# Kernel tuning notes

Hardware: AMD Instinct MI355X
Metric: run time of the kernel (lower is better)

## Reference

```python
import jax, jax.numpy as jnp
import numpy as np

DIM = 768
N_HEADS = 12
HEAD_DIM = DIM // N_HEADS
B, S = 16, 1024


def setup_inputs() -> dict:
    key = jax.random.key(0)
    k1, k2, k3, k4, k5 = jax.random.split(key, 5)
    scale = 0.02
    return {
        "x": jax.random.normal(k1, (B, S, DIM), dtype=jnp.float32),
        "W_attn": jax.random.normal(k2, (DIM, 3 * DIM), dtype=jnp.float32) * scale,
        "b_attn": jnp.zeros((3 * DIM,), dtype=jnp.float32),
        "W_proj": jax.random.normal(k3, (DIM, DIM), dtype=jnp.float32) * scale,
        "b_proj": jnp.zeros((DIM,), dtype=jnp.float32),
    }


def reference(x, W_attn, b_attn, W_proj, b_proj):
    # Dropout layers act as identity (eval mode) for a deterministic reference.
    Bsz, Sq, D = x.shape
    qkv = x @ W_attn + b_attn                      # [B, S, 3D]
    q, k, v = jnp.split(qkv, 3, axis=-1)
    q = q.reshape(Bsz, Sq, N_HEADS, HEAD_DIM)
    k = k.reshape(Bsz, Sq, N_HEADS, HEAD_DIM)
    v = v.reshape(Bsz, Sq, N_HEADS, HEAD_DIM)
    # scores: [B, H, S, S]
    w = jnp.einsum('bqhd,bkhd->bhqk', q, k) / jnp.sqrt(jnp.float32(HEAD_DIM))
    causal = jnp.tril(jnp.ones((Sq, Sq), dtype=bool))
    mask_value = jnp.finfo(w.dtype).min
    w = jnp.where(causal[None, None], w, mask_value)
    w = jax.nn.softmax(w, axis=-1)
    attn = jnp.einsum('bhqk,bkhd->bqhd', w, v).reshape(Bsz, Sq, D)
    return attn @ W_proj + b_proj
```

## Files before the change

### kernel.cpp

```cpp
#include <hip/hip_runtime.h>
#include <hip/hip_bf16.h>
#include <math.h>

#define BDIM 16
#define SEQ 1024
#define DIM 768
#define NH 12
#define HD 64
#define M_ROWS (BDIM * SEQ)
#define N_QKV (3 * DIM)
#define QN (BDIM * NH * SEQ * HD)

typedef __attribute__((ext_vector_type(8))) short bf16x8_t;
typedef __attribute__((ext_vector_type(4))) float f32x4_t;
typedef __attribute__((ext_vector_type(16))) float f32x16_t;
typedef __attribute__((ext_vector_type(4))) unsigned int u32x4_t;

__device__ __forceinline__ unsigned short f2bf(float x) {
    return __builtin_bit_cast(unsigned short, __float2bfloat16(x));
}

__device__ __forceinline__ void gld_lds16(const void* g, void* l) {
    __builtin_amdgcn_global_load_lds(
        (const __attribute__((address_space(1))) void*)g,
        (__attribute__((address_space(3))) void*)l, 16, 0, 0);
}

__device__ __forceinline__ unsigned int cvt_pk_bf16(float a, float b) {
    unsigned int r;
    asm("v_cvt_pk_bf16_f32 %0, %1, %2" : "=v"(r) : "v"(a), "v"(b));
    return r;
}

__device__ __forceinline__ void perm32swap(unsigned int& a, unsigned int& b) {
    asm("v_permlane32_swap_b32 %0, %1" : "+v"(a), "+v"(b));
}

#define QSCALE 0.18033688011112042f

#define X_BLOCKS 6144
#define WA_TILES 432
#define WP_TILES 144

__global__ __launch_bounds__(256) void prep(
    const float* __restrict__ x, const float* __restrict__ Wa,
    const float* __restrict__ Wp,
    unsigned short* __restrict__ xb, unsigned short* __restrict__ Wat,
    unsigned short* __restrict__ Wpt)
{
    __shared__ unsigned short T[64][72];
    const int bid = blockIdx.x;
    const int tid = threadIdx.x;

    if (bid < X_BLOCKS) {
        size_t base = (size_t)bid * 2048 + tid * 8;
        float4 f0 = *(const float4*)&x[base];
        float4 f1 = *(const float4*)&x[base + 4];
        unsigned short tmp[8] = {f2bf(f0.x), f2bf(f0.y), f2bf(f0.z), f2bf(f0.w),
                                 f2bf(f1.x), f2bf(f1.y), f2bf(f1.z), f2bf(f1.w)};
        *(uint4*)&xb[base] = *(uint4*)tmp;
        return;
    }
    const float* W; unsigned short* Wt; int N, kt, nt;
    int b2 = bid - X_BLOCKS;
    if (b2 < WA_TILES) { W = Wa; Wt = Wat; N = N_QKV; kt = b2 / 36; nt = b2 % 36; }
    else { b2 -= WA_TILES; W = Wp; Wt = Wpt; N = DIM; kt = b2 / 12; nt = b2 % 12; }
    const int k0 = kt * 64, n0 = nt * 64;
#pragma unroll
    for (int c = 0; c < 4; c++) {
        int idx = c * 256 + tid;
        int r = idx >> 4;
        int c4 = (idx & 15) * 4;
        float4 v = *(const float4*)&W[(size_t)(k0 + r) * N + n0 + c4];
        T[r][c4 + 0] = f2bf(v.x);
        T[r][c4 + 1] = f2bf(v.y);
        T[r][c4 + 2] = f2bf(v.z);
        T[r][c4 + 3] = f2bf(v.w);
    }
    __syncthreads();
#pragma unroll
    for (int c = 0; c < 2; c++) {
        int idx = c * 256 + tid;
        int n = idx >> 3;
        int ch = (idx & 7) * 8;
        unsigned short tmp[8];
#pragma unroll
        for (int j = 0; j < 8; j++) tmp[j] = T[ch + j][n];
        *(uint4*)&Wt[(size_t)(n0 + n) * DIM + k0 + ch] = *(uint4*)tmp;
    }
}

__global__ __launch_bounds__(256, 2) void gemm_qkv_mfma(
    const unsigned short* __restrict__ Ab,
    const unsigned short* __restrict__ Bt,
    const float* __restrict__ bias,
    unsigned short* __restrict__ Qo, unsigned short* __restrict__ Ko,
    unsigned short* __restrict__ Vt)
{
    __shared__ unsigned short smem[32768];

    const int tid = threadIdx.x;
    const int lane = tid & 63;
    const int w = tid >> 6;
    const int wm = w >> 1, wn = w & 1;
    const int ln = lane & 15, quad = lane >> 4;
    const int bm = blockIdx.y * 128, bn = blockIdx.x * 128;

    f32x4_t acc[4][4];
#pragma unroll
    for (int i = 0; i < 4; i++)
#pragma unroll
        for (int j = 0; j < 4; j++) acc[i][j] = (f32x4_t){0.f, 0.f, 0.f, 0.f};

#pragma unroll
    for (int c = 0; c < 4; c++) {
        int idx = c * 256 + tid;
        int r = idx >> 3;
        int gch = (idx & 7) ^ (r & 7);
        gld_lds16(&Ab[(size_t)(bm + r) * DIM + gch * 8], &smem[idx * 8]);
        gld_lds16(&Bt[(size_t)(bn + r) * DIM + gch * 8], &smem[8192 + idx * 8]);
    }

    for (int ki = 0; ki < 12; ki++) {
        __syncthreads();
        unsigned short* As = smem + (ki & 1) * 16384;
        unsigned short* Bs = As + 8192;

        if (ki < 11) {
            const int nk0 = (ki + 1) * 64;
            unsigned short* Asn = smem + ((ki + 1) & 1) * 16384;
            unsigned short* Bsn = Asn + 8192;
#pragma unroll
            for (int c = 0; c < 4; c++) {
                int idx = c * 256 + tid;
                int r = idx >> 3;
                int gch = (idx & 7) ^ (r & 7);
                gld_lds16(&Ab[(size_t)(bm + r) * DIM + nk0 + gch * 8], &Asn[idx * 8]);
                gld_lds16(&Bt[(size_t)(bn + r) * DIM + nk0 + gch * 8], &Bsn[idx * 8]);
            }
        }

#pragma unroll
        for (int kk = 0; kk < 2; kk++) {
            bf16x8_t af[4], bfr[4];
#pragma unroll
            for (int mt = 0; mt < 4; mt++) {
                int r = wm * 64 + mt * 16 + ln;
                int c = (kk * 4 + quad) ^ (ln & 7);
                af[mt] = *(const bf16x8_t*)&As[r * 64 + c * 8];
            }
#pragma unroll
            for (int nt = 0; nt < 4; nt++) {
                int r = wn * 64 + nt * 16 + ln;
                int c = (kk * 4 + quad) ^ (ln & 7);
                bfr[nt] = *(const bf16x8_t*)&Bs[r * 64 + c * 8];
            }
#pragma unroll
            for (int mt = 0; mt < 4; mt++)
#pragma unroll
                for (int nt = 0; nt < 4; nt++)
                    acc[mt][nt] = __builtin_amdgcn_mfma_f32_16x16x32_bf16(
                        af[mt], bfr[nt], acc[mt][nt], 0, 0, 0);
        }
    }
    __syncthreads();

    const int nb = bn + wn * 64;
    const int part = nb / DIM;
    const int h = (nb % DIM) >> 6;
    const float scale = (part == 0) ? QSCALE : 1.0f;
    const int mb = bm + wm * 64;
    const int b_ = mb >> 10;
    const int s0 = mb & 1023;
    unsigned short* Wb = smem + w * 4608;

    float bias_v[4];
#pragma unroll
    for (int nt = 0; nt < 4; nt++) bias_v[nt] = bias[nb + nt * 16 + ln];

    if (part < 2) {
#pragma unroll
        for (int mt = 0; mt < 4; mt++)
#pragma unroll
            for (int nt = 0; nt < 4; nt++)
#pragma unroll
                for (int r = 0; r < 4; r++)
                    Wb[(mt * 16 + quad * 4 + r) * 72 + nt * 16 + ln] =
                        f2bf((acc[mt][nt][r] + bias_v[nt]) * scale);
        unsigned short* dst = (part == 0) ? Qo : Ko;
        size_t obase = (((size_t)b_ * NH + h) * SEQ + s0) * HD;
#pragma unroll
        for (int c = 0; c < 8; c++) {
            int idx = c * 64 + lane;
            int rr = idx >> 3;
            int ch = (idx & 7) * 8;
            *(uint4*)&dst[obase + (size_t)rr * HD + ch] = *(uint4*)&Wb[rr * 72 + ch];
        }
    } else {
#pragma unroll
        for (int mt = 0; mt < 4; mt++)
#pragma unroll
            for (int nt = 0; nt < 4; nt++)
#pragma unroll
                for (int r = 0; r < 4; r++)
                    Wb[(nt * 16 + ln) * 72 + mt * 16 + quad * 4 + r] =
                        f2bf(acc[mt][nt][r] + bias_v[nt]);
        size_t obase = ((size_t)b_ * NH + h) * (size_t)HD * SEQ;
#pragma unroll
        for (int c = 0; c < 8; c++) {
            int idx = c * 64 + lane;
            int d = idx >> 3;
            int ch = (idx & 7) * 8;
            *(uint4*)&Vt[obase + (size_t)d * SEQ + s0 + ch] = *(uint4*)&Wb[d * 72 + ch];
        }
    }
}

__global__ __launch_bounds__(256, 2) void gemm_proj_mfma(
    const unsigned short* __restrict__ Ab,
    const unsigned short* __restrict__ Bt,
    const float* __restrict__ bias,
    float* __restrict__ C)
{
    __shared__ unsigned short smem[32768];

    const int tid = threadIdx.x;
    const int lane = tid & 63;
    const int w = tid >> 6;
    const int wm = w >> 1, wn = w & 1;
    const int ln = lane & 15, quad = lane >> 4;
    const int bm = blockIdx.y * 128, bn = blockIdx.x * 128;

    f32x4_t acc[4][4];
#pragma unroll
    for (int i = 0; i < 4; i++)
#pragma unroll
        for (int j = 0; j < 4; j++) acc[i][j] = (f32x4_t){0.f, 0.f, 0.f, 0.f};

#pragma unroll
    for (int c = 0; c < 4; c++) {
        int idx = c * 256 + tid;
        int r = idx >> 3;
        int gch = (idx & 7) ^ (r & 7);
        gld_lds16(&Ab[(size_t)(bm + r) * DIM + gch * 8], &smem[idx * 8]);
        gld_lds16(&Bt[(size_t)(bn + r) * DIM + gch * 8], &smem[8192 + idx * 8]);
    }

    for (int ki = 0; ki < 12; ki++) {
        __syncthreads();
        unsigned short* As = smem + (ki & 1) * 16384;
        unsigned short* Bs = As + 8192;

        if (ki < 11) {
            const int nk0 = (ki + 1) * 64;
            unsigned short* Asn = smem + ((ki + 1) & 1) * 16384;
            unsigned short* Bsn = Asn + 8192;
#pragma unroll
            for (int c = 0; c < 4; c++) {
                int idx = c * 256 + tid;
                int r = idx >> 3;
                int gch = (idx & 7) ^ (r & 7);
                gld_lds16(&Ab[(size_t)(bm + r) * DIM + nk0 + gch * 8], &Asn[idx * 8]);
                gld_lds16(&Bt[(size_t)(bn + r) * DIM + nk0 + gch * 8], &Bsn[idx * 8]);
            }
        }

#pragma unroll
        for (int kk = 0; kk < 2; kk++) {
            bf16x8_t af[4], bfr[4];
#pragma unroll
            for (int mt = 0; mt < 4; mt++) {
                int r = wm * 64 + mt * 16 + ln;
                int c = (kk * 4 + quad) ^ (ln & 7);
                af[mt] = *(const bf16x8_t*)&As[r * 64 + c * 8];
            }
#pragma unroll
            for (int nt = 0; nt < 4; nt++) {
                int r = wn * 64 + nt * 16 + ln;
                int c = (kk * 4 + quad) ^ (ln & 7);
                bfr[nt] = *(const bf16x8_t*)&Bs[r * 64 + c * 8];
            }
#pragma unroll
            for (int mt = 0; mt < 4; mt++)
#pragma unroll
                for (int nt = 0; nt < 4; nt++)
                    acc[mt][nt] = __builtin_amdgcn_mfma_f32_16x16x32_bf16(
                        af[mt], bfr[nt], acc[mt][nt], 0, 0, 0);
        }
    }

    const int nb = bn + wn * 64;
    float bias_v[4];
#pragma unroll
    for (int nt = 0; nt < 4; nt++) bias_v[nt] = bias[nb + nt * 16 + ln];
#pragma unroll
    for (int mt = 0; mt < 4; mt++)
#pragma unroll
        for (int nt = 0; nt < 4; nt++)
#pragma unroll
            for (int r = 0; r < 4; r++) {
                int m = bm + wm * 64 + mt * 16 + quad * 4 + r;
                C[(size_t)m * DIM + nb + nt * 16 + ln] = acc[mt][nt][r] + bias_v[nt];
            }
}

__global__ __launch_bounds__(256, 3) void attn_mfma(
    const unsigned short* __restrict__ Qg, const unsigned short* __restrict__ Kg,
    const unsigned short* __restrict__ Vt, unsigned short* __restrict__ Out)
{
    __shared__ unsigned short Ks[2][4096];
    __shared__ unsigned short Vs[2][4096];

    const int tid = threadIdx.x;
    const int lane = tid & 63;
    const int w = tid >> 6;
    const int wpair = w >> 1;
    const int whigh = w & 1;
    const int l31 = lane & 31;
    const int hi = lane >> 5;
    const int l7 = lane & 7;

    const int bh = blockIdx.y;
    const size_t gbase = (size_t)bh * SEQ * HD;
    const int b_ = bh / NH;
    const int h = bh % NH;

    for (int ph = 0; ph < 2; ph++) {
        const int qt = ph ? blockIdx.x : 7 - blockIdx.x;
        const int qbase = qt * 128;
        const int ntiles = 2 * qt + 2;
        const int wtiles = 2 * qt + 1 + wpair;
        const int qr0 = qbase + w * 32;

        bf16x8_t aq[4];
#pragma unroll
        for (int ds = 0; ds < 4; ds++)
            aq[ds] = *(const bf16x8_t*)
                &Qg[gbase + (size_t)(qr0 + l31) * HD + ds * 16 + hi * 8];

        f32x16_t acc[2];
#pragma unroll
        for (int dh = 0; dh < 2; dh++)
#pragma unroll
            for (int j = 0; j < 16; j++) acc[dh][j] = 0.f;
        float lsum = 0.f;

        __syncthreads();

#pragma unroll
        for (int i = 0; i < 2; i++) {
            int idx = i * 256 + tid;
            int r = idx >> 3;
            int gc = (idx & 7) ^ (r & 7);
            gld_lds16(&Kg[gbase + (size_t)r * HD + gc * 8], &Ks[0][idx * 8]);
            gld_lds16(&Vt[gbase + (size_t)r * SEQ + gc * 8], &Vs[0][idx * 8]);
        }

        for (int t = 0; t < ntiles; t++) {
            __syncthreads();
            const int cur = t & 1;

            if (t + 1 < ntiles) {
                const int nk0 = (t + 1) * 64;
#pragma unroll
                for (int i = 0; i < 2; i++) {
                    int idx = i * 256 + tid;
                    int r = idx >> 3;
                    int gc = (idx & 7) ^ (r & 7);
                    gld_lds16(&Kg[gbase + (size_t)(nk0 + r) * HD + gc * 8],
                              &Ks[cur ^ 1][idx * 8]);
                    gld_lds16(&Vt[gbase + (size_t)r * SEQ + nk0 + gc * 8],
                              &Vs[cur ^ 1][idx * 8]);
                }
            }
            if (t >= wtiles) continue;
            const bool diag = (t == 2 * qt + wpair);
            const int kgend = diag ? (1 + whigh) : 2;

            for (int kg = 0; kg < kgend; kg++) {
                bf16x8_t kf[4];
#pragma unroll
                for (int ds = 0; ds < 4; ds++)
                    kf[ds] = *(const bf16x8_t*)
                        &Ks[cur][(kg * 32 + l31) * 64 + (((ds * 2 + hi) ^ l7) * 8)];

                f32x16_t sa;
#pragma unroll
                for (int j = 0; j < 16; j++) sa[j] = 0.f;
                __builtin_amdgcn_s_setprio(1);
#pragma unroll
                for (int ds = 0; ds < 4; ds++)
                    sa = __builtin_amdgcn_mfma_f32_32x32x16_bf16(
                        kf[ds], aq[ds], sa, 0, 0, 0);
                __builtin_amdgcn_s_setprio(0);

                const bool dm = diag && (kg == whigh);
                const int qr = qr0 + l31;
                float p[16];
#pragma unroll
                for (int j = 0; j < 16; j++) {
                    float pv = exp2f(sa[j]);
                    if (dm) {
                        int key = t * 64 + kg * 32 + (j & 3) + 8 * (j >> 2) + 4 * hi;
                        if (key > qr) pv = 0.f;
                    }
                    lsum += pv;
                    p[j] = pv;
                }
                unsigned int c0 = cvt_pk_bf16(p[0], p[1]);
                unsigned int c1 = cvt_pk_bf16(p[2], p[3]);
                unsigned int c2 = cvt_pk_bf16(p[4], p[5]);
                unsigned int c3 = cvt_pk_bf16(p[6], p[7]);
                unsigned int c4 = cvt_pk_bf16(p[8], p[9]);
                unsigned int c5 = cvt_pk_bf16(p[10], p[11]);
                unsigned int c6 = cvt_pk_bf16(p[12], p[13]);
                unsigned int c7 = cvt_pk_bf16(p[14], p[15]);
                perm32swap(c0, c2);
                perm32swap(c1, c3);
                perm32swap(c4, c6);
                perm32swap(c5, c7);
                u32x4_t u0, u1;
                u0[0] = c0; u0[1] = c1; u0[2] = c2; u0[3] = c3;
                u1[0] = c4; u1[1] = c5; u1[2] = c6; u1[3] = c7;
                bf16x8_t pa0 = __builtin_bit_cast(bf16x8_t, u0);
                bf16x8_t pa1 = __builtin_bit_cast(bf16x8_t, u1);

                __builtin_amdgcn_s_setprio(1);
#pragma unroll
                for (int dh = 0; dh < 2; dh++) {
                    bf16x8_t vf0 = *(const bf16x8_t*)
                        &Vs[cur][(dh * 32 + l31) * 64 +
                                 (((kg * 4 + 0 + hi) ^ l7) * 8)];
                    acc[dh] = __builtin_amdgcn_mfma_f32_32x32x16_bf16(
                        pa0, vf0, acc[dh], 0, 0, 0);
                    bf16x8_t vf1 = *(const bf16x8_t*)
                        &Vs[cur][(dh * 32 + l31) * 64 +
                                 (((kg * 4 + 2 + hi) ^ l7) * 8)];
                    acc[dh] = __builtin_amdgcn_mfma_f32_32x32x16_bf16(
                        pa1, vf1, acc[dh], 0, 0, 0);
                }
                __builtin_amdgcn_s_setprio(0);
            }
        }

        lsum += __shfl_xor(lsum, 32);

        float rin[16];
#pragma unroll
        for (int j = 0; j < 16; j++)
            rin[j] = 1.0f / __shfl(lsum, (j & 3) + 8 * (j >> 2) + 4 * hi);
#pragma unroll
        for (int dh = 0; dh < 2; dh++)
#pragma unroll
            for (int j = 0; j < 16; j++) {
                int row = qr0 + (j & 3) + 8 * (j >> 2) + 4 * hi;
                Out[((size_t)b_ * SEQ + row) * DIM + h * HD + dh * 32 + l31] =
                    f2bf(acc[dh][j] * rin[j]);
            }
    }
}

extern "C" void kernel_launch(void* const* d_in, const int* in_sizes, int n_in,
                              void* d_out, int out_size, void* d_ws, size_t ws_size,
                              hipStream_t stream) {
    const float* x  = (const float*)d_in[0];
    const float* Wa = (const float*)d_in[1];
    const float* ba = (const float*)d_in[2];
    const float* Wp = (const float*)d_in[3];
    const float* bp = (const float*)d_in[4];
    float* out = (float*)d_out;

    unsigned short* ws = (unsigned short*)d_ws;
    unsigned short* Qg  = ws;
    unsigned short* Kg  = Qg + (size_t)QN;
    unsigned short* Vt  = Kg + (size_t)QN;
    unsigned short* xb  = Vt + (size_t)QN;
    unsigned short* AO  = xb + (size_t)QN;
    unsigned short* Wat = AO + (size_t)QN;
    unsigned short* Wpt = Wat + (size_t)(N_QKV * DIM);

    prep<<<X_BLOCKS + WA_TILES + WP_TILES, 256, 0, stream>>>(
        x, Wa, Wp, xb, Wat, Wpt);

    dim3 g_qkv(N_QKV / 128, M_ROWS / 128);
    gemm_qkv_mfma<<<g_qkv, 256, 0, stream>>>(xb, Wat, ba, Qg, Kg, Vt);

    dim3 g_attn(4, BDIM * NH);
    attn_mfma<<<g_attn, 256, 0, stream>>>(Qg, Kg, Vt, AO);

    dim3 g_proj(DIM / 128, M_ROWS / 128);
    gemm_proj_mfma<<<g_proj, 256, 0, stream>>>(AO, Wpt, bp, out);
}
```

Measured before the change: 271.6 us.

## Remap blocks across XCDs, compute softmax row sums via MFMA, refine LDS swizzle

Adds an XCD-aware block remapping to the QKV GEMM, projection GEMM and attention kernels so that neighbouring tiles land on the same XCD and share L2. In attention, the per-lane scalar row-sum plus shuffle reduction is replaced by an extra MFMA against a vector of bf16 ones. exp2f becomes a raw v_exp_f32, and the K/V LDS swizzle adds a row-group XOR term to cut bank conflicts. The attention output buffer now reuses the xb workspace, which lowers the memory footprint. The ones-MFMA sums bf16-rounded probabilities rather than fp32 ones, a small numeric difference.

```diff
diff --git a/kernel.cpp b/kernel.cpp
--- a/kernel.cpp
+++ b/kernel.cpp
@@ -34,6 +34,16 @@
 
 __device__ __forceinline__ void perm32swap(unsigned int& a, unsigned int& b) {
     asm("v_permlane32_swap_b32 %0, %1" : "+v"(a), "+v"(b));
+}
+
+__device__ __forceinline__ float exp2_fast(float x) {
+    float r;
+    asm("v_exp_f32 %0, %1" : "=v"(r) : "v"(x));
+    return r;
+}
+
+__device__ __forceinline__ int xcd_remap(int lin, int chunk) {
+    return (lin & 7) * chunk + (lin >> 3);
 }
 
 #define QSCALE 0.18033688011112042f
@@ -104,7 +114,9 @@
     const int w = tid >> 6;
     const int wm = w >> 1, wn = w & 1;
     const int ln = lane & 15, quad = lane >> 4;
-    const int bm = blockIdx.y * 128, bn = blockIdx.x * 128;
+    const int lin = blockIdx.x + 18 * blockIdx.y;
+    const int jj = xcd_remap(lin, 288);
+    const int bm = (jj / 18) * 128, bn = (jj % 18) * 128;
 
     f32x4_t acc[4][4];
 #pragma unroll
@@ -229,7 +241,9 @@
     const int w = tid >> 6;
     const int wm = w >> 1, wn = w & 1;
     const int ln = lane & 15, quad = lane >> 4;
-    const int bm = blockIdx.y * 128, bn = blockIdx.x * 128;
+    const int lin = blockIdx.x + 6 * blockIdx.y;
+    const int jj = xcd_remap(lin, 96);
+    const int bm = (jj / 6) * 128, bn = (jj % 6) * 128;
 
     f32x4_t acc[4][4];
 #pragma unroll
@@ -303,6 +317,8 @@
                 C[(size_t)m * DIM + nb + nt * 16 + ln] = acc[mt][nt][r] + bias_v[nt];
             }
 }
+
+#define SWZ(r) ((((r) & 7)) ^ ((((r) >> 3)) & 3))
 
 __global__ __launch_bounds__(256, 3) void attn_mfma(
     const unsigned short* __restrict__ Qg, const unsigned short* __restrict__ Kg,
@@ -319,14 +335,22 @@
     const int l31 = lane & 31;
     const int hi = lane >> 5;
     const int l7 = lane & 7;
-
-    const int bh = blockIdx.y;
+    const int sw3 = (l31 >> 3) & 3;
+
+    const int lin = blockIdx.x + 4 * blockIdx.y;
+    const int jj = xcd_remap(lin, 96);
+    const int bxn = jj & 3;
+    const int bh = jj >> 2;
     const size_t gbase = (size_t)bh * SEQ * HD;
     const int b_ = bh / NH;
     const int h = bh % NH;
 
+    bf16x8_t vones;
+#pragma unroll
+    for (int i = 0; i < 8; i++) vones[i] = (short)0x3F80;
+
     for (int ph = 0; ph < 2; ph++) {
-        const int qt = ph ? blockIdx.x : 7 - blockIdx.x;
+        const int qt = ph ? bxn : 7 - bxn;
         const int qbase = qt * 128;
         const int ntiles = 2 * qt + 2;
         const int wtiles = 2 * qt + 1 + wpair;
@@ -339,11 +363,11 @@
                 &Qg[gbase + (size_t)(qr0 + l31) * HD + ds * 16 + hi * 8];
 
         f32x16_t acc[2];
-#pragma unroll
-        for (int dh = 0; dh < 2; dh++)
-#pragma unroll
-            for (int j = 0; j < 16; j++) acc[dh][j] = 0.f;
-        float lsum = 0.f;
+        f32x16_t lacc;
+#pragma unroll
+        for (int j = 0; j < 16; j++) {
+            acc[0][j] = 0.f; acc[1][j] = 0.f; lacc[j] = 0.f;
+        }
 
         __syncthreads();
 
@@ -351,7 +375,7 @@
         for (int i = 0; i < 2; i++) {
             int idx = i * 256 + tid;
             int r = idx >> 3;
-            int gc = (idx & 7) ^ (r & 7);
+            int gc = (idx & 7) ^ SWZ(r);
             gld_lds16(&Kg[gbase + (size_t)r * HD + gc * 8], &Ks[0][idx * 8]);
             gld_lds16(&Vt[gbase + (size_t)r * SEQ + gc * 8], &Vs[0][idx * 8]);
         }
@@ -366,7 +390,7 @@
                 for (int i = 0; i < 2; i++) {
                     int idx = i * 256 + tid;
                     int r = idx >> 3;
-                    int gc = (idx & 7) ^ (r & 7);
+                    int gc = (idx & 7) ^ SWZ(r);
                     gld_lds16(&Kg[gbase + (size_t)(nk0 + r) * HD + gc * 8],
                               &Ks[cur ^ 1][idx * 8]);
                     gld_lds16(&Vt[gbase + (size_t)r * SEQ + nk0 + gc * 8],
@@ -382,7 +406,8 @@
 #pragma unroll
                 for (int ds = 0; ds < 4; ds++)
                     kf[ds] = *(const bf16x8_t*)
-                        &Ks[cur][(kg * 32 + l31) * 64 + (((ds * 2 + hi) ^ l7) * 8)];
+                        &Ks[cur][(kg * 32 + l31) * 64 +
+                                 (((ds * 2 + hi) ^ l7 ^ sw3) * 8)];
 
                 f32x16_t sa;
 #pragma unroll
@@ -399,12 +424,11 @@
                 float p[16];
 #pragma unroll
                 for (int j = 0; j < 16; j++) {
-                    float pv = exp2f(sa[j]);
+                    float pv = exp2_fast(sa[j]);
                     if (dm) {
                         int key = t * 64 + kg * 32 + (j & 3) + 8 * (j >> 2) + 4 * hi;
                         if (key > qr) pv = 0.f;
                     }
-                    lsum += pv;
                     p[j] = pv;
                 }
                 unsigned int c0 = cvt_pk_bf16(p[0], p[1]);
@@ -426,16 +450,20 @@
                 bf16x8_t pa1 = __builtin_bit_cast(bf16x8_t, u1);
 
                 __builtin_amdgcn_s_setprio(1);
+                lacc = __builtin_amdgcn_mfma_f32_32x32x16_bf16(
+                    pa0, vones, lacc, 0, 0, 0);
+                lacc = __builtin_amdgcn_mfma_f32_32x32x16_bf16(
+                    pa1, vones, lacc, 0, 0, 0);
 #pragma unroll
                 for (int dh = 0; dh < 2; dh++) {
                     bf16x8_t vf0 = *(const bf16x8_t*)
                         &Vs[cur][(dh * 32 + l31) * 64 +
-                                 (((kg * 4 + 0 + hi) ^ l7) * 8)];
+                                 (((kg * 4 + 0 + hi) ^ l7 ^ sw3) * 8)];
                     acc[dh] = __builtin_amdgcn_mfma_f32_32x32x16_bf16(
                         pa0, vf0, acc[dh], 0, 0, 0);
                     bf16x8_t vf1 = *(const bf16x8_t*)
                         &Vs[cur][(dh * 32 + l31) * 64 +
-                                 (((kg * 4 + 2 + hi) ^ l7) * 8)];
+                                 (((kg * 4 + 2 + hi) ^ l7 ^ sw3) * 8)];
                     acc[dh] = __builtin_amdgcn_mfma_f32_32x32x16_bf16(
                         pa1, vf1, acc[dh], 0, 0, 0);
                 }
@@ -443,12 +471,9 @@
             }
         }
 
-        lsum += __shfl_xor(lsum, 32);
-
         float rin[16];
 #pragma unroll
-        for (int j = 0; j < 16; j++)
-            rin[j] = 1.0f / __shfl(lsum, (j & 3) + 8 * (j >> 2) + 4 * hi);
+        for (int j = 0; j < 16; j++) rin[j] = 1.0f / lacc[j];
 #pragma unroll
         for (int dh = 0; dh < 2; dh++)
 #pragma unroll
@@ -475,8 +500,8 @@
     unsigned short* Kg  = Qg + (size_t)QN;
     unsigned short* Vt  = Kg + (size_t)QN;
     unsigned short* xb  = Vt + (size_t)QN;
-    unsigned short* AO  = xb + (size_t)QN;
-    unsigned short* Wat = AO + (size_t)QN;
+    unsigned short* AO  = xb;
+    unsigned short* Wat = xb + (size_t)QN;
     unsigned short* Wpt = Wat + (size_t)(N_QKV * DIM);
 
     prep<<<X_BLOCKS + WA_TILES + WP_TILES, 256, 0, stream>>>(
```

Result: faster. 239.0 us (-12.0%).
